# Kernel optimization log

Hardware: AMD Instinct MI355X
Metric: run time of the kernel (lower is better)

Reference implementation:

```python
import jax, jax.numpy as jnp
import numpy as np

N_RAYS = 131072          # rays in batch (e.g., 512x256 tile)
N_SAMPLES = 4194304      # total occupied samples after occ-grid culling (~32/ray)
STEP = 5e-3              # render_step_size (from render_step_size_vals)


def setup_inputs() -> dict:
    key = jax.random.key(0)
    k1, k2, k3, k4 = jax.random.split(key, 4)
    # sorted ray indices, as produced by occGrid.sampling (packed, ascending)
    ray_indices = jnp.sort(jax.random.randint(k1, (N_SAMPLES,), 0, N_RAYS)).astype(jnp.int32)
    t_starts = jax.random.uniform(k2, (N_SAMPLES,), jnp.float32) * 4.0
    t_ends = t_starts + STEP
    sigmas = jax.random.uniform(k3, (N_SAMPLES,), jnp.float32) * 50.0  # raw densities (density_scale=1)
    hdr = jax.random.uniform(k4, (N_SAMPLES, 3), jnp.float32)          # per-sample HDR radiance
    return {"t_starts": t_starts, "t_ends": t_ends, "sigmas": sigmas,
            "hdr": hdr, "ray_indices": ray_indices, "n_rays": N_RAYS}


def _render_and_accumulate(t_starts, t_ends, sigmas, hdr, ray_indices, n_rays):
    S = t_starts.shape[0]
    dt = t_ends - t_starts
    sdt = sigmas * dt                              # sigma * delta_t per sample
    alphas = 1.0 - jnp.exp(-sdt)                   # per-sample alpha
    # exclusive per-ray cumsum of sdt: global exclusive cumsum minus value at segment lead
    excl = jnp.cumsum(sdt) - sdt                   # global exclusive cumsum
    flag = jnp.concatenate([jnp.ones((1,), bool), ray_indices[1:] != ray_indices[:-1]])
    # index of the lead (first) sample of each ray segment, propagated forward
    lead = jax.lax.associative_scan(jnp.maximum, jnp.where(flag, jnp.arange(S), 0))
    trans = jnp.exp(-(excl - excl[lead]))          # transmittance T_i within each ray
    weights = trans * alphas                       # render_weight_from_density
    # accumulate_along_rays (segment reduce); indices are sorted
    opac = jax.ops.segment_sum(weights, ray_indices, num_segments=n_rays,
                               indices_are_sorted=True)                      # [n_rays]
    hdr_acc = jax.ops.segment_sum(weights[:, None] * hdr, ray_indices,
                                  num_segments=n_rays, indices_are_sorted=True)  # [n_rays,3]
    return jnp.concatenate([opac[:, None], hdr_acc], axis=-1)  # [n_rays, 4] = (opacity, hdr)


def reference(t_starts, t_ends, sigmas, hdr, ray_indices, n_rays):
    return _render_and_accumulate(t_starts, t_ends, sigmas, hdr, ray_indices, n_rays)
```

## Files before the change

### kernel.cpp

```cpp
#include <hip/hip_runtime.h>


#define TPB 256
#define LDSF (256 * 17)

#define DPP0(SRC, CTRL, RMASK, BC) __int_as_float(__builtin_amdgcn_update_dpp( \
        0, __float_as_int(SRC), (CTRL), (RMASK), 0xf, (BC)))

__device__ __forceinline__ float fold16_dpp(float x) {
    float a = 0.0f;
    a = __fadd_rn(a, DPP0(x, 0x110 | 15, 0xf, true));
    a = __fadd_rn(a, DPP0(x, 0x110 | 14, 0xf, true));
    a = __fadd_rn(a, DPP0(x, 0x110 | 13, 0xf, true));
    a = __fadd_rn(a, DPP0(x, 0x110 | 12, 0xf, true));
    a = __fadd_rn(a, DPP0(x, 0x110 | 11, 0xf, true));
    a = __fadd_rn(a, DPP0(x, 0x110 | 10, 0xf, true));
    a = __fadd_rn(a, DPP0(x, 0x110 |  9, 0xf, true));
    a = __fadd_rn(a, DPP0(x, 0x110 |  8, 0xf, true));
    a = __fadd_rn(a, DPP0(x, 0x110 |  7, 0xf, true));
    a = __fadd_rn(a, DPP0(x, 0x110 |  6, 0xf, true));
    a = __fadd_rn(a, DPP0(x, 0x110 |  5, 0xf, true));
    a = __fadd_rn(a, DPP0(x, 0x110 |  4, 0xf, true));
    a = __fadd_rn(a, DPP0(x, 0x110 |  3, 0xf, true));
    a = __fadd_rn(a, DPP0(x, 0x110 |  2, 0xf, true));
    a = __fadd_rn(a, DPP0(x, 0x110 |  1, 0xf, true));
    a = __fadd_rn(a, x);
    return a;
}

__device__ __forceinline__ float wscan(float v) {
    v = __fadd_rn(v, DPP0(v, 0x111, 0xf, true));
    v = __fadd_rn(v, DPP0(v, 0x112, 0xf, true));
    v = __fadd_rn(v, DPP0(v, 0x114, 0xf, true));
    v = __fadd_rn(v, DPP0(v, 0x118, 0xf, true));
    v = __fadd_rn(v, DPP0(v, 0x142, 0xa, false));
    v = __fadd_rn(v, DPP0(v, 0x143, 0xc, false));
    return v;
}

__device__ __forceinline__ float sdt_c(float tsv, float tev, float sgv) {
    return __fmul_rn(sgv, __fsub_rn(tev, tsv));
}

__global__ void k_bottom(const float* __restrict__ ts, const float* __restrict__ te,
                         const float* __restrict__ sg, int S,
                         float* __restrict__ sdt, float* __restrict__ s1,
                         float* __restrict__ T1,
                         float4* __restrict__ out4, int n_rays) {
    __shared__ float lds[LDSF];
    int t = threadIdx.x;
    int tile = blockIdx.x;
    int gid = tile * TPB + t;
    if (gid < n_rays) out4[gid] = make_float4(0.f, 0.f, 0.f, 0.f);
    const float4* ts4 = (const float4*)ts;
    const float4* te4 = (const float4*)te;
    const float4* sg4 = (const float4*)sg;
    float4* sdt4 = (float4*)sdt;
    #pragma unroll
    for (int k = 0; k < 4; ++k) {
        int idx4 = tile * 1024 + k * 256 + t;
        float4 a = ts4[idx4], b = te4[idx4], c = sg4[idx4];
        float4 xo;
        xo.x = sdt_c(a.x, b.x, c.x);
        xo.y = sdt_c(a.y, b.y, c.y);
        xo.z = sdt_c(a.z, b.z, c.z);
        xo.w = sdt_c(a.w, b.w, c.w);
        sdt4[idx4] = xo;
        int fl = (k * 256 + t) << 2;
        int g0 = fl >> 4, j0 = fl & 15;
        float* p = &lds[g0 * 17 + j0];
        p[0] = xo.x; p[1] = xo.y; p[2] = xo.z; p[3] = xo.w;
    }
    __syncthreads();
    float acc = 0.0f;
    #pragma unroll
    for (int j = 0; j < 16; ++j) acc = __fadd_rn(acc, lds[t * 17 + j]);
    float acc2 = fold16_dpp(acc);
    int g = tile * 256 + t;
    s1[g] = acc2;
    if ((t & 15) == 15) T1[g >> 4] = acc2;
}

__global__ void k_mid(const float* __restrict__ T1, float* __restrict__ C2) {
    __shared__ float T2sh[1024];
    __shared__ float s3sh[1024];
    __shared__ float s4sh[64];
    __shared__ float T3sh[64];
    __shared__ float T4sh[4];
    __shared__ float C5sh[4];
    int t = threadIdx.x;
    const float4* T14 = (const float4*)T1;
    float s2l[16];
    float acc = 0.0f;
    #pragma unroll
    for (int k = 0; k < 4; ++k) {
        float4 v = T14[t * 4 + k];
        acc = __fadd_rn(acc, v.x); s2l[k * 4 + 0] = acc;
        acc = __fadd_rn(acc, v.y); s2l[k * 4 + 1] = acc;
        acc = __fadd_rn(acc, v.z); s2l[k * 4 + 2] = acc;
        acc = __fadd_rn(acc, v.w); s2l[k * 4 + 3] = acc;
    }
    T2sh[t] = acc;
    __syncthreads();
    if (t < 64) {
        float a3 = 0.0f;
        for (int j = 0; j < 16; ++j) { a3 = __fadd_rn(a3, T2sh[t * 16 + j]); s3sh[t * 16 + j] = a3; }
        T3sh[t] = a3;
    }
    __syncthreads();
    if (t < 4) {
        float a4 = 0.0f;
        for (int j = 0; j < 16; ++j) { a4 = __fadd_rn(a4, T3sh[t * 16 + j]); s4sh[t * 16 + j] = a4; }
        T4sh[t] = a4;
    }
    __syncthreads();
    if (t == 0) {
        float c = 0.0f;
        for (int r = 0; r < 4; ++r) { c = __fadd_rn(c, T4sh[r]); C5sh[r] = c; }
    }
    __syncthreads();
    if (t < 64) {
        int r = t >> 4;
        float v4 = s4sh[t];
        s4sh[t] = r ? __fadd_rn(v4, C5sh[r - 1]) : v4;
    }
    __syncthreads();
    {
        int r = t >> 4;
        float v3 = s3sh[t];
        float c3 = r ? __fadd_rn(v3, s4sh[r - 1]) : v3;
        s3sh[t] = c3;
    }
    __syncthreads();
    float c3m = t ? s3sh[t - 1] : 0.0f;
    float4* C24 = (float4*)C2;
    #pragma unroll
    for (int k = 0; k < 4; ++k) {
        float4 o;
        o.x = t ? __fadd_rn(s2l[k * 4 + 0], c3m) : s2l[k * 4 + 0];
        o.y = t ? __fadd_rn(s2l[k * 4 + 1], c3m) : s2l[k * 4 + 1];
        o.z = t ? __fadd_rn(s2l[k * 4 + 2], c3m) : s2l[k * 4 + 2];
        o.w = t ? __fadd_rn(s2l[k * 4 + 3], c3m) : s2l[k * 4 + 3];
        C24[t * 4 + k] = o;
    }
}

__global__ void k_render(const int* __restrict__ ri, const float* __restrict__ sdt,
                         const float* __restrict__ s1, const float* __restrict__ C2,
                         const float* __restrict__ hdr,
                         int S, float* __restrict__ out) {
    int t = threadIdx.x & 63;
    int i = blockIdx.x * TPB + threadIdx.x;
    int wb = i - t;
    bool valid = i < S;
    float x = valid ? sdt[i] : 0.0f;
    int r  = valid ? ri[i] : (-1 - t);
    int pr = valid ? ((i == 0) ? (r ^ 1) : ri[i - 1]) : -1000;

    bool f = (pr != r);
    unsigned long long mask = __ballot(f);

    float acc = fold16_dpp(x);

    int g = i >> 4;
    float Ci = acc;
    if (g) {
        int j = g - 1;
        float cj = (j >> 4) ? __fadd_rn(s1[j], C2[(j >> 4) - 1]) : s1[j];
        Ci = __fadd_rn(acc, cj);
    }
    float excl = __fsub_rn(Ci, x);

    unsigned long long bits_le = mask & (~0ull >> (63 - t));
    float el_lead = 0.0f;
    if (!(mask & 1ull)) {
        int r0 = __builtin_amdgcn_readfirstlane(r);
        int h0 = 0;
        for (int round = 0; round < 65536; ++round) {
            int idx = wb - 1 - t - 64 * round;
            int rv = (idx >= 0) ? ri[idx] : (r0 ^ 1);
            unsigned long long mm = __ballot(rv != r0);
            if (mm) {
                int lm = __ffsll((unsigned long long)mm) - 1;
                h0 = wb - 64 * round - lm;
                break;
            }
        }
        float elv = 0.0f;
        if (t == 0) {
            const float4* s4 = (const float4*)sdt;
            int gh = h0 >> 4, lh = h0 & 15;
            float4 q0 = s4[gh * 4 + 0], q1 = s4[gh * 4 + 1];
            float4 q2 = s4[gh * 4 + 2], q3 = s4[gh * 4 + 3];
            float vv[16] = { q0.x, q0.y, q0.z, q0.w, q1.x, q1.y, q1.z, q1.w,
                             q2.x, q2.y, q2.z, q2.w, q3.x, q3.y, q3.z, q3.w };
            float a2 = 0.0f, xl = 0.0f;
            #pragma unroll
            for (int j2 = 0; j2 < 16; ++j2) {
                if (j2 <= lh) { a2 = __fadd_rn(a2, vv[j2]); xl = vv[j2]; }
            }
            float Ch = a2;
            if (gh) {
                int j3 = gh - 1;
                float cj = (j3 >> 4) ? __fadd_rn(s1[j3], C2[(j3 >> 4) - 1]) : s1[j3];
                Ch = __fadd_rn(a2, cj);
            }
            elv = __fsub_rn(Ch, xl);
        }
        el_lead = __int_as_float(__builtin_amdgcn_readfirstlane(__float_as_int(elv)));
    }

    int h = bits_le ? (63 - __clzll((long long)bits_le)) : 0;
    int esrc = bits_le ? h : t;
    float elh = __shfl(excl, esrc, 64);
    float el = bits_le ? elh : el_lead;

    float w = 0.0f, hr = 0.0f, hg = 0.0f, hb = 0.0f;
    if (valid) {
        float expo  = __fsub_rn(excl, el);
        float trans = __expf(-expo);
        float alpha = __fsub_rn(1.0f, __expf(-x));
        w  = __fmul_rn(trans, alpha);
        hr = hdr[3 * i + 0]; hg = hdr[3 * i + 1]; hb = hdr[3 * i + 2];
    }

    float4 sc;
    sc.x = wscan(w);
    sc.y = wscan(__fmul_rn(w, hr));
    sc.z = wscan(__fmul_rn(w, hg));
    sc.w = wscan(__fmul_rn(w, hb));

    int bsrc = (h > 0) ? (h - 1) : t;
    float4 bs;
    bs.x = __shfl(sc.x, bsrc, 64);
    bs.y = __shfl(sc.y, bsrc, 64);
    bs.z = __shfl(sc.z, bsrc, 64);
    bs.w = __shfl(sc.w, bsrc, 64);
    if (h == 0) { bs.x = 0.f; bs.y = 0.f; bs.z = 0.f; bs.w = 0.f; }

    bool nf = (t < 63) ? (((mask >> (t + 1)) & 1ull) != 0ull) : true;
    if (valid && nf && r >= 0) {
        float* o = out + 4 * r;
        atomicAdd(o + 0, sc.x - bs.x);
        atomicAdd(o + 1, sc.y - bs.y);
        atomicAdd(o + 2, sc.z - bs.z);
        atomicAdd(o + 3, sc.w - bs.w);
    }
}

extern "C" void kernel_launch(void* const* d_in, const int* in_sizes, int n_in,
                              void* d_out, int out_size, void* d_ws, size_t ws_size,
                              hipStream_t stream) {
    const float* ts  = (const float*)d_in[0];
    const float* te  = (const float*)d_in[1];
    const float* sg  = (const float*)d_in[2];
    const float* hdr = (const float*)d_in[3];
    const int*   ri  = (const int*)d_in[4];
    const int S      = in_sizes[0];
    const int n_rays = out_size / 4;
    const int N1 = S >> 4;
    const int N2 = N1 >> 4;

    char* w = (char*)d_ws;
    auto alloc = [&](size_t bytes) { char* p = w; w += (bytes + 255) & ~255ULL; return p; };
    float* sdt = (float*)alloc((size_t)S * 4);
    float* s1  = (float*)alloc((size_t)N1 * 4);
    float* T1  = (float*)alloc((size_t)N2 * 4);
    float* C2  = (float*)alloc((size_t)N2 * 4);

    k_bottom<<<dim3(N1 / TPB), dim3(TPB), 0, stream>>>(ts, te, sg, S, sdt, s1, T1,
                                                       (float4*)d_out, n_rays);
    k_mid   <<<dim3(1), dim3(1024), 0, stream>>>(T1, C2);
    k_render<<<dim3((S + TPB - 1) / TPB), dim3(TPB), 0, stream>>>(ri, sdt, s1, C2, hdr, S, (float*)d_out);
}
```

Measured before the change: 177.0 us.

## Process four samples per thread in render kernel with vectorized loads

The render kernel now has each thread handle four consecutive samples. It uses float4/int4 loads for sdt, ray indices and hdr, and runs a serial in-thread prefix combined with a DPP carry across each 4-lane group. Segment-head lookup is rebuilt as a max-scan over lane keys, and per-segment sums come from the wave scan of thread-level totals. This is meant to cut the launch size, the scalar and strided hdr loads, and the number of wave scans per sample. In exchange it adds more register pressure and branching, and assumes S is divisible by 1024.

```diff
diff --git a/kernel.cpp b/kernel.cpp
--- a/kernel.cpp
+++ b/kernel.cpp
@@ -6,6 +6,10 @@
 
 #define DPP0(SRC, CTRL, RMASK, BC) __int_as_float(__builtin_amdgcn_update_dpp( \
         0, __float_as_int(SRC), (CTRL), (RMASK), 0xf, (BC)))
+
+#define IMAXD(V, CTRL, RMASK, BC) { \
+    int _tmp = __builtin_amdgcn_update_dpp(0, (V), (CTRL), (RMASK), 0xf, (BC)); \
+    (V) = ((V) > _tmp) ? (V) : _tmp; }
 
 __device__ __forceinline__ float fold16_dpp(float x) {
     float a = 0.0f;
@@ -149,40 +153,74 @@
                          const float* __restrict__ s1, const float* __restrict__ C2,
                          const float* __restrict__ hdr,
                          int S, float* __restrict__ out) {
-    int t = threadIdx.x & 63;
-    int i = blockIdx.x * TPB + threadIdx.x;
-    int wb = i - t;
-    bool valid = i < S;
-    float x = valid ? sdt[i] : 0.0f;
-    int r  = valid ? ri[i] : (-1 - t);
-    int pr = valid ? ((i == 0) ? (r ^ 1) : ri[i - 1]) : -1000;
-
-    bool f = (pr != r);
-    unsigned long long mask = __ballot(f);
-
-    float acc = fold16_dpp(x);
-
-    int g = i >> 4;
-    float Ci = acc;
-    if (g) {
-        int j = g - 1;
-        float cj = (j >> 4) ? __fadd_rn(s1[j], C2[(j >> 4) - 1]) : s1[j];
-        Ci = __fadd_rn(acc, cj);
-    }
-    float excl = __fsub_rn(Ci, x);
-
-    unsigned long long bits_le = mask & (~0ull >> (63 - t));
+    const int tid = blockIdx.x * TPB + threadIdx.x;
+    const int t = threadIdx.x & 63;
+    const int i0 = tid * 4;
+    const bool valid = i0 < S;
+
+    float4 xq = valid ? ((const float4*)sdt)[tid] : make_float4(0.f, 0.f, 0.f, 0.f);
+    int4 rq;
+    if (valid) rq = ((const int4*)ri)[tid];
+    else { rq.x = rq.y = rq.z = rq.w = -1 - t; }
+
+    int dpr = __builtin_amdgcn_update_dpp(0, rq.w, 0x111, 0xf, 0xf, true);
+    int prev_r = dpr;
+    if ((t & 15) == 0) prev_r = (i0 == 0 || !valid) ? (rq.x ^ 1) : ri[i0 - 1];
+
+    bool f0 = prev_r != rq.x;
+    bool f1 = rq.y != rq.x;
+    bool f2 = rq.z != rq.y;
+    bool f3 = rq.w != rq.z;
+    unsigned long long mask0 = __ballot(f0);
+
+    int q = t & 3;
+    float p0 = __fadd_rn(0.0f, xq.x);
+    float p1 = __fadd_rn(p0, xq.y);
+    float p2 = __fadd_rn(p1, xq.z);
+    float p3 = __fadd_rn(p2, xq.w);
+    float pf = p3;
+    #pragma unroll
+    for (int rr = 1; rr <= 3; ++rr) {
+        float cin = DPP0(pf, 0x111, 0xf, true);
+        float n0 = __fadd_rn(cin, xq.x);
+        float n1 = __fadd_rn(n0, xq.y);
+        float n2 = __fadd_rn(n1, xq.z);
+        float n3 = __fadd_rn(n2, xq.w);
+        bool me = (q == rr);
+        p0 = me ? n0 : p0;
+        p1 = me ? n1 : p1;
+        p2 = me ? n2 : p2;
+        p3 = me ? n3 : p3;
+        pf = me ? n3 : pf;
+    }
+
+    int g = i0 >> 4;
+    float cj = 0.0f;
+    if (valid && g) {
+        int j3 = g - 1;
+        cj = (j3 >> 4) ? __fadd_rn(s1[j3], C2[(j3 >> 4) - 1]) : s1[j3];
+    }
+    float C0 = g ? __fadd_rn(p0, cj) : p0;
+    float C1v = g ? __fadd_rn(p1, cj) : p1;
+    float C2v = g ? __fadd_rn(p2, cj) : p2;
+    float C3v = g ? __fadd_rn(p3, cj) : p3;
+    float e0 = __fsub_rn(C0, xq.x);
+    float e1 = __fsub_rn(C1v, xq.y);
+    float e2 = __fsub_rn(C2v, xq.z);
+    float e3 = __fsub_rn(C3v, xq.w);
+
     float el_lead = 0.0f;
-    if (!(mask & 1ull)) {
-        int r0 = __builtin_amdgcn_readfirstlane(r);
+    if (!(mask0 & 1ull)) {
+        int wbs = (tid - t) * 4;
+        int r0v = __builtin_amdgcn_readfirstlane(rq.x);
         int h0 = 0;
         for (int round = 0; round < 65536; ++round) {
-            int idx = wb - 1 - t - 64 * round;
-            int rv = (idx >= 0) ? ri[idx] : (r0 ^ 1);
-            unsigned long long mm = __ballot(rv != r0);
+            int idx = wbs - 1 - t - 64 * round;
+            int rv = (idx >= 0) ? ri[idx] : (r0v ^ 1);
+            unsigned long long mm = __ballot(rv != r0v);
             if (mm) {
                 int lm = __ffsll((unsigned long long)mm) - 1;
-                h0 = wb - 64 * round - lm;
+                h0 = wbs - 64 * round - lm;
                 break;
             }
         }
@@ -201,50 +239,124 @@
             }
             float Ch = a2;
             if (gh) {
-                int j3 = gh - 1;
-                float cj = (j3 >> 4) ? __fadd_rn(s1[j3], C2[(j3 >> 4) - 1]) : s1[j3];
-                Ch = __fadd_rn(a2, cj);
+                int j3b = gh - 1;
+                float cjb = (j3b >> 4) ? __fadd_rn(s1[j3b], C2[(j3b >> 4) - 1]) : s1[j3b];
+                Ch = __fadd_rn(a2, cjb);
             }
             elv = __fsub_rn(Ch, xl);
         }
         el_lead = __int_as_float(__builtin_amdgcn_readfirstlane(__float_as_int(elv)));
     }
 
-    int h = bits_le ? (63 - __clzll((long long)bits_le)) : 0;
-    int esrc = bits_le ? h : t;
-    float elh = __shfl(excl, esrc, 64);
-    float el = bits_le ? elh : el_lead;
-
-    float w = 0.0f, hr = 0.0f, hg = 0.0f, hb = 0.0f;
+    int lh0 = f0 ? 0 : -1;
+    int lh1 = f1 ? 1 : lh0;
+    int lh2 = f2 ? 2 : lh1;
+    int lh3 = f3 ? 3 : lh2;
+
+    int key = (lh3 >= 0) ? (t + 1) : 0;
+    int sk = __shfl_up(key, 1, 64);
+    if (t == 0) sk = 0;
+    int M = sk;
+    IMAXD(M, 0x111, 0xf, true)
+    IMAXD(M, 0x112, 0xf, true)
+    IMAXD(M, 0x114, 0xf, true)
+    IMAXD(M, 0x118, 0xf, true)
+    IMAXD(M, 0x142, 0xa, false)
+    IMAXD(M, 0x143, 0xc, false)
+    int src = M;
+    int psrc = (src > 0) ? (src - 1) : t;
+
+    float el_last = (lh3 == 3) ? e3 : (lh3 == 2) ? e2 : (lh3 == 1) ? e1 : e0;
+    float rel = __shfl(el_last, psrc, 64);
+    float el_prev = (src > 0) ? rel : el_lead;
+
+    float el0 = (lh0 >= 0) ? e0 : el_prev;
+    float el1 = (lh1 == 1) ? e1 : ((lh1 == 0) ? e0 : el_prev);
+    float el2 = (lh2 == 2) ? e2 : ((lh2 == 1) ? e1 : ((lh2 == 0) ? e0 : el_prev));
+    float el3 = (lh3 == 3) ? e3 : ((lh3 == 2) ? e2 : ((lh3 == 1) ? e1 :
+                ((lh3 == 0) ? e0 : el_prev)));
+
+    float4 h0v, h1v, h2v;
     if (valid) {
-        float expo  = __fsub_rn(excl, el);
-        float trans = __expf(-expo);
-        float alpha = __fsub_rn(1.0f, __expf(-x));
-        w  = __fmul_rn(trans, alpha);
-        hr = hdr[3 * i + 0]; hg = hdr[3 * i + 1]; hb = hdr[3 * i + 2];
-    }
-
-    float4 sc;
-    sc.x = wscan(w);
-    sc.y = wscan(__fmul_rn(w, hr));
-    sc.z = wscan(__fmul_rn(w, hg));
-    sc.w = wscan(__fmul_rn(w, hb));
-
-    int bsrc = (h > 0) ? (h - 1) : t;
-    float4 bs;
-    bs.x = __shfl(sc.x, bsrc, 64);
-    bs.y = __shfl(sc.y, bsrc, 64);
-    bs.z = __shfl(sc.z, bsrc, 64);
-    bs.w = __shfl(sc.w, bsrc, 64);
-    if (h == 0) { bs.x = 0.f; bs.y = 0.f; bs.z = 0.f; bs.w = 0.f; }
-
-    bool nf = (t < 63) ? (((mask >> (t + 1)) & 1ull) != 0ull) : true;
-    if (valid && nf && r >= 0) {
-        float* o = out + 4 * r;
-        atomicAdd(o + 0, sc.x - bs.x);
-        atomicAdd(o + 1, sc.y - bs.y);
-        atomicAdd(o + 2, sc.z - bs.z);
-        atomicAdd(o + 3, sc.w - bs.w);
+        const float4* h4 = (const float4*)hdr;
+        h0v = h4[3 * tid + 0]; h1v = h4[3 * tid + 1]; h2v = h4[3 * tid + 2];
+    } else {
+        h0v = h1v = h2v = make_float4(0.f, 0.f, 0.f, 0.f);
+    }
+    float w0 = 0.f, w1 = 0.f, w2 = 0.f, w3 = 0.f;
+    if (valid) {
+        w0 = __fmul_rn(__expf(-__fsub_rn(e0, el0)), __fsub_rn(1.0f, __expf(-xq.x)));
+        w1 = __fmul_rn(__expf(-__fsub_rn(e1, el1)), __fsub_rn(1.0f, __expf(-xq.y)));
+        w2 = __fmul_rn(__expf(-__fsub_rn(e2, el2)), __fsub_rn(1.0f, __expf(-xq.z)));
+        w3 = __fmul_rn(__expf(-__fsub_rn(e3, el3)), __fsub_rn(1.0f, __expf(-xq.w)));
+    }
+    float4 v0 = make_float4(w0, __fmul_rn(w0, h0v.x), __fmul_rn(w0, h0v.y), __fmul_rn(w0, h0v.z));
+    float4 v1 = make_float4(w1, __fmul_rn(w1, h0v.w), __fmul_rn(w1, h1v.x), __fmul_rn(w1, h1v.y));
+    float4 v2 = make_float4(w2, __fmul_rn(w2, h1v.z), __fmul_rn(w2, h1v.w), __fmul_rn(w2, h2v.x));
+    float4 v3 = make_float4(w3, __fmul_rn(w3, h2v.y), __fmul_rn(w3, h2v.z), __fmul_rn(w3, h2v.w));
+
+    float4 V0 = v0;
+    float4 V1 = make_float4(V0.x + v1.x, V0.y + v1.y, V0.z + v1.z, V0.w + v1.w);
+    float4 V2 = make_float4(V1.x + v2.x, V1.y + v2.y, V1.z + v2.z, V1.w + v2.w);
+    float4 V3 = make_float4(V2.x + v3.x, V2.y + v3.y, V2.z + v3.z, V2.w + v3.w);
+
+    float4 W;
+    W.x = wscan(V3.x); W.y = wscan(V3.y); W.z = wscan(V3.z); W.w = wscan(V3.w);
+    float4 E;
+    E.x = __shfl_up(W.x, 1, 64);
+    E.y = __shfl_up(W.y, 1, 64);
+    E.z = __shfl_up(W.z, 1, 64);
+    E.w = __shfl_up(W.w, 1, 64);
+    if (t == 0) { E.x = 0.f; E.y = 0.f; E.z = 0.f; E.w = 0.f; }
+
+    float4 Vm1 = (lh3 == 1) ? V0 : ((lh3 == 2) ? V1 : V2);
+    float4 bs_last;
+    if (lh3 > 0) {
+        bs_last = make_float4(E.x + Vm1.x, E.y + Vm1.y, E.z + Vm1.z, E.w + Vm1.w);
+    } else {
+        bs_last = E;
+    }
+    float4 rbs;
+    rbs.x = __shfl(bs_last.x, psrc, 64);
+    rbs.y = __shfl(bs_last.y, psrc, 64);
+    rbs.z = __shfl(bs_last.z, psrc, 64);
+    rbs.w = __shfl(bs_last.w, psrc, 64);
+    float4 bs_prev = (src > 0) ? rbs : make_float4(0.f, 0.f, 0.f, 0.f);
+
+    bool t0 = f1, t1 = f2, t2 = f3;
+    bool t3 = (t < 63) ? (((mask0 >> (t + 1)) & 1ull) != 0ull) : true;
+
+    if (valid) {
+        #pragma unroll
+        for (int j = 0; j < 4; ++j) {
+            bool tl = (j == 0) ? t0 : (j == 1) ? t1 : (j == 2) ? t2 : t3;
+            if (!tl) continue;
+            int lhj = (j == 0) ? lh0 : (j == 1) ? lh1 : (j == 2) ? lh2 : lh3;
+            float4 Vj = (j == 0) ? V0 : (j == 1) ? V1 : (j == 2) ? V2 : V3;
+            int rj = (j == 0) ? rq.x : (j == 1) ? rq.y : (j == 2) ? rq.z : rq.w;
+            float4 bsj;
+            if (lhj >= 0) {
+                if (lhj > 0) {
+                    float4 Vh = (lhj == 1) ? V0 : ((lhj == 2) ? V1 : V2);
+                    bsj = make_float4(E.x + Vh.x, E.y + Vh.y, E.z + Vh.z, E.w + Vh.w);
+                } else {
+                    bsj = E;
+                }
+            } else {
+                bsj = bs_prev;
+            }
+            float px = (E.x + Vj.x) - bsj.x;
+            float py = (E.y + Vj.y) - bsj.y;
+            float pz = (E.z + Vj.z) - bsj.z;
+            float pw = (E.w + Vj.w) - bsj.w;
+            if (rj >= 0) {
+                float* o = out + 4 * rj;
+                atomicAdd(o + 0, px);
+                atomicAdd(o + 1, py);
+                atomicAdd(o + 2, pz);
+                atomicAdd(o + 3, pw);
+            }
+        }
     }
 }
 
@@ -271,5 +383,5 @@
     k_bottom<<<dim3(N1 / TPB), dim3(TPB), 0, stream>>>(ts, te, sg, S, sdt, s1, T1,
                                                        (float4*)d_out, n_rays);
     k_mid   <<<dim3(1), dim3(1024), 0, stream>>>(T1, C2);
-    k_render<<<dim3((S + TPB - 1) / TPB), dim3(TPB), 0, stream>>>(ri, sdt, s1, C2, hdr, S, (float*)d_out);
-}
+    k_render<<<dim3(S / (TPB * 4)), dim3(TPB), 0, stream>>>(ri, sdt, s1, C2, hdr, S, (float*)d_out);
+}
```

After: 164.9 us. -6.8%, faster.
